# Optimization experiments

Measured on AMD Instinct MI355X. Metric: run time of the kernel, lower is better.

Reference implementation:

```python
import jax, jax.numpy as jnp
import numpy as np

B, T, C = 4, 4096, 1024
DEGREE, EXPAND = 2, 2
H = EXPAND * C  # selector / inner dim = 2048


def setup_inputs() -> dict:
    key = jax.random.key(0)
    ks = jax.random.split(key, 4)
    sc = lambda d: 1.0 / np.sqrt(d)
    return {
        "x": jax.random.normal(ks[0], (B, T, C), jnp.float32),
        "W_sel": jax.random.normal(ks[1], (C, H), jnp.float32) * sc(C),
        "W_agg": jax.random.normal(ks[2], (C, DEGREE * H), jnp.float32) * sc(C),
        "W_out": jax.random.normal(ks[3], (H, C), jnp.float32) * sc(H),
        "sqk_q": jnp.ones((H,), jnp.float32),
        "sqk_k": jnp.ones((DEGREE * H,), jnp.float32),
    }


def reference(x, W_sel, W_agg, W_out, sqk_q, sqk_k):
    # Selector branch on queries (gated): B,T,H
    s = jax.nn.silu(jnp.einsum('btc,ch->bth', x, W_sel) * sqk_q)
    # Aggregator branch on context: B,T,DEGREE*H
    h = jnp.einsum('btc,cd->btd', x, W_agg) * sqk_k
    chunks = jnp.split(h, DEGREE, axis=-1)
    # Polynomial expansion: sum_{d=1..DEGREE} prod_{k<=d} chunk_k  -> B,T,H
    p = chunks[0]
    poly = p
    for c in chunks[1:]:
        p = p * c
        poly = poly + p
    # Causal masked mean: tril(ones(T,T)) @ poly / row-count == cumsum / arange.
    # Honors the causal structure without materializing the T x T mask.
    denom = jnp.arange(1, T + 1, dtype=poly.dtype)[None, :, None]
    agg = jnp.cumsum(poly, axis=1) / denom  # B,T,H causal running mean
    # Mix selected queries with aggregated polynomial state, project out.
    return jnp.einsum('bth,hc->btc', s * agg, W_out)
```

## Files before the change

### kernel.cpp

```cpp
#include <hip/hip_runtime.h>
#include <hip/hip_bf16.h>
#include <stdint.h>

#define BB 4
#define TT 4096
#define CC 1024
#define HH 2048
#define MM (BB*TT)
#define NCK 32
#define CKS 128

using short8 = __attribute__((ext_vector_type(8))) short;
using f32x4  = __attribute__((ext_vector_type(4))) float;

__device__ __forceinline__ unsigned short f2bf(float f) {
    union { float f; uint32_t u; } v; v.f = f;
    uint32_t r = v.u + 0x7fffu + ((v.u >> 16) & 1u);
    return (unsigned short)(r >> 16);
}
__device__ __forceinline__ float bf_lo(uint32_t u) {
    union { uint32_t u; float f; } v; v.u = u << 16; return v.f;
}
__device__ __forceinline__ float bf_hi(uint32_t u) {
    union { uint32_t u; float f; } v; v.u = u & 0xFFFF0000u; return v.f;
}
__device__ __forceinline__ uint32_t pack2bf(float lo, float hi) {
    return ((uint32_t)f2bf(lo)) | (((uint32_t)f2bf(hi)) << 16);
}

__global__ void conv_x_kernel(const float* __restrict__ x, unsigned short* __restrict__ xb, int n4) {
    int i = blockIdx.x * blockDim.x + threadIdx.x;
    if (i >= n4) return;
    float4 v = ((const float4*)x)[i];
    ushort4 o;
    o.x = f2bf(v.x); o.y = f2bf(v.y); o.z = f2bf(v.z); o.w = f2bf(v.w);
    ((ushort4*)xb)[i] = o;
}

__global__ void trans_direct_kernel(const float* __restrict__ in, unsigned short* __restrict__ out,
                                    const float* __restrict__ scale, int R, int Cin) {
    __shared__ float tile[32][33];
    int c0 = blockIdx.x * 32, k0 = blockIdx.y * 32;
    int tx = threadIdx.x;
    for (int i = threadIdx.y; i < 32; i += 8) {
        float s = scale ? scale[c0 + tx] : 1.f;
        tile[i][tx] = in[(size_t)(k0 + i) * Cin + c0 + tx] * s;
    }
    __syncthreads();
    for (int i = threadIdx.y; i < 32; i += 8)
        out[(size_t)(c0 + i) * R + k0 + tx] = f2bf(tile[tx][i]);
}

__global__ void trans_pair_kernel(const float* __restrict__ in, unsigned short* __restrict__ out,
                                  const float* __restrict__ scale) {
    __shared__ float tile[32][33];
    int q0 = blockIdx.x * 32, k0 = blockIdx.y * 32;
    int g = q0 >> 5;
    int tx = threadIdx.x;
    int c = (tx < 16) ? (g * 16 + tx) : (2048 + g * 16 + tx - 16);
    float s = scale[c];
    for (int i = threadIdx.y; i < 32; i += 8)
        tile[i][tx] = in[(size_t)(k0 + i) * 4096 + c] * s;
    __syncthreads();
    for (int i = threadIdx.y; i < 32; i += 8)
        out[(size_t)(q0 + i) * 1024 + k0 + tx] = f2bf(tile[tx][i]);
}

template<int LDK, int NT>
__device__ __forceinline__ void gemm_core(
    const unsigned short* __restrict__ A,
    const unsigned short* __restrict__ Bt,
    int m0, int n0, int tid,
    f32x4 (&acc)[8][4])
{
    __shared__ __align__(16) unsigned short As[3 * 4096];
    __shared__ __align__(16) unsigned short Bs[3 * 8192];

    const int lane = tid & 63;
    const int l15  = lane & 15;
    const int quad = lane >> 4;
    const int wn   = (tid >> 6) << 6;

#pragma unroll
    for (int i = 0; i < 8; i++)
#pragma unroll
        for (int j = 0; j < 4; j++) acc[i][j] = {0.f, 0.f, 0.f, 0.f};

    const int rl  = tid >> 2;
    const int kc8 = ((tid & 3) ^ ((tid >> 3) & 3)) << 3;
    const unsigned short* gA = A  + (size_t)(m0 + rl) * LDK + kc8;
    const unsigned short* gB = Bt + (size_t)(n0 + rl) * LDK + kc8;

#define STAGE(G, L) __builtin_amdgcn_global_load_lds( \
        (const __attribute__((address_space(1))) void*)(G), \
        (__attribute__((address_space(3))) void*)(L), 16, 0, 0)
#define SWZ(row) ((quad ^ (((row) >> 1) & 3)) << 3)

#pragma unroll
    for (int t = 0; t < 2; t++) {
        STAGE(gA + t * 32,                    &As[t * 4096 + tid * 8]);
        STAGE(gA + 64 * (size_t)LDK + t * 32, &As[t * 4096 + 2048 + tid * 8]);
#pragma unroll
        for (int u = 0; u < 4; u++)
            STAGE(gB + (size_t)(u * 64) * LDK + t * 32, &Bs[t * 8192 + u * 2048 + tid * 8]);
    }
    asm volatile("s_waitcnt vmcnt(6)" ::: "memory");
    __builtin_amdgcn_s_barrier();

    unsigned short* aC = As;            unsigned short* bC = Bs;
    unsigned short* aN = As + 4096;     unsigned short* bN = Bs + 8192;
    unsigned short* aS = As + 8192;     unsigned short* bS = Bs + 16384;

    for (int t = 0; t < NT; ++t) {
        const bool pf = (t + 2) < NT;

        short8 af[4], bf[4];
#pragma unroll
        for (int i = 0; i < 4; i++) {
            int row = i * 16 + l15;
            af[i] = *(const short8*)(aC + row * 32 + SWZ(row));
        }
#pragma unroll
        for (int j = 0; j < 4; j++) {
            int row = wn + j * 16 + l15;
            bf[j] = *(const short8*)(bC + row * 32 + SWZ(row));
        }
        if (pf) {
            STAGE(gA + (size_t)(t + 2) * 32,                    aS + tid * 8);
            STAGE(gA + 64 * (size_t)LDK + (size_t)(t + 2) * 32, aS + 2048 + tid * 8);
        }
        __builtin_amdgcn_s_barrier();
        asm volatile("s_waitcnt lgkmcnt(0)" ::: "memory");
        __builtin_amdgcn_sched_barrier(0);
        __builtin_amdgcn_s_setprio(1);
#pragma unroll
        for (int i = 0; i < 4; i++)
#pragma unroll
            for (int j = 0; j < 4; j++)
                acc[i][j] = __builtin_amdgcn_mfma_f32_16x16x32_bf16(af[i], bf[j], acc[i][j], 0, 0, 0);
        __builtin_amdgcn_s_setprio(0);
        __builtin_amdgcn_sched_barrier(0);
        __builtin_amdgcn_s_barrier();

        short8 ag[4];
#pragma unroll
        for (int i = 0; i < 4; i++) {
            int row = 64 + i * 16 + l15;
            ag[i] = *(const short8*)(aC + row * 32 + SWZ(row));
        }
        if (pf) {
#pragma unroll
            for (int u = 0; u < 4; u++)
                STAGE(gB + (size_t)(u * 64) * LDK + (size_t)(t + 2) * 32, bS + u * 2048 + tid * 8);
        }
        __builtin_amdgcn_s_barrier();
        asm volatile("s_waitcnt lgkmcnt(0)" ::: "memory");
        __builtin_amdgcn_sched_barrier(0);
        __builtin_amdgcn_s_setprio(1);
#pragma unroll
        for (int i = 0; i < 4; i++)
#pragma unroll
            for (int j = 0; j < 4; j++)
                acc[4 + i][j] = __builtin_amdgcn_mfma_f32_16x16x32_bf16(ag[i], bf[j], acc[4 + i][j], 0, 0, 0);
        __builtin_amdgcn_s_setprio(0);
        __builtin_amdgcn_sched_barrier(0);
        if (t < NT - 2) { asm volatile("s_waitcnt vmcnt(6)" ::: "memory"); }
        else            { asm volatile("s_waitcnt vmcnt(0)" ::: "memory"); }
        __builtin_amdgcn_s_barrier();

        unsigned short* ta = aC; aC = aN; aN = aS; aS = ta;
        unsigned short* tb = bC; bC = bN; bN = bS; bS = tb;
    }
#undef STAGE
#undef SWZ
}

__global__ __launch_bounds__(256, 2) void gemm_fused_kernel(
    const unsigned short* __restrict__ A,
    const unsigned short* __restrict__ Bt,
    unsigned short* __restrict__ Sout,
    unsigned short* __restrict__ Pout,
    float* __restrict__ part)
{
    __shared__ float psum[128];
    const int tid = threadIdx.x;
    const int xcd = blockIdx.x & 7;
    const int j   = blockIdx.x >> 3;
    const int mt  = j / 3;
    const int nt  = xcd * 3 + (j % 3);
    const int m0 = mt << 7, n0 = nt << 8;
    if (tid < 128) psum[tid] = 0.f;

    f32x4 acc[8][4];
    gemm_core<1024, 32>(A, Bt, m0, n0, tid, acc);

    const int lane = tid & 63;
    const int l15  = lane & 15;
    const int quad = lane >> 4;
    const int wn   = (tid >> 6) << 6;

    if (nt < 8) {
#pragma unroll
        for (int i = 0; i < 8; i++)
#pragma unroll
            for (int j2 = 0; j2 < 4; j2++) {
                int col = n0 + wn + j2 * 16 + l15;
#pragma unroll
                for (int r = 0; r < 4; r++) {
                    int row = m0 + i * 16 + quad * 4 + r;
                    float v = acc[i][j2][r];
                    v = v / (1.f + __expf(-v));
                    Sout[(size_t)row * 2048 + col] = f2bf(v);
                }
            }
    } else {
        const int pbase = ((n0 - 2048 + wn) >> 1);
        float lsum0 = 0.f, lsum1 = 0.f;
#pragma unroll
        for (int i = 0; i < 8; i++) {
#pragma unroll
            for (int jp = 0; jp < 2; jp++) {
                int pcol = pbase + jp * 16 + l15;
#pragma unroll
                for (int r = 0; r < 4; r++) {
                    int row = m0 + i * 16 + quad * 4 + r;
                    float pv = acc[i][2 * jp][r] * (1.f + acc[i][2 * jp + 1][r]);
                    Pout[(size_t)row * 2048 + pcol] = f2bf(pv);
                    if (jp == 0) lsum0 += pv; else lsum1 += pv;
                }
            }
        }
        int base = (wn >> 1) + l15;
        atomicAdd(&psum[base], lsum0);
        atomicAdd(&psum[base + 16], lsum1);
        __syncthreads();
        if (tid < 128) {
            int b  = m0 >> 12;
            int ck = (m0 & 4095) >> 7;
            part[((size_t)b * NCK + ck) * 2048 + ((n0 - 2048) >> 1) + tid] = psum[tid];
        }
    }
}

__global__ __launch_bounds__(256, 2) void gemm_out_kernel(
    const unsigned short* __restrict__ A,
    const unsigned short* __restrict__ Bt,
    float* __restrict__ Cout)
{
    const int tid = threadIdx.x;
    const int xcd = blockIdx.x & 7;
    const int j   = blockIdx.x >> 3;
    const int nt  = xcd >> 1;
    const int mt  = (xcd & 1) * 64 + j;
    const int m0 = mt << 7, n0 = nt << 8;

    f32x4 acc[8][4];
    gemm_core<2048, 64>(A, Bt, m0, n0, tid, acc);

    const int lane = tid & 63;
    const int l15  = lane & 15;
    const int quad = lane >> 4;
    const int wn   = (tid >> 6) << 6;
#pragma unroll
    for (int i = 0; i < 8; i++)
#pragma unroll
        for (int j2 = 0; j2 < 4; j2++) {
            int col = n0 + wn + j2 * 16 + l15;
#pragma unroll
            for (int r = 0; r < 4; r++) {
                int row = m0 + i * 16 + quad * 4 + r;
                Cout[(size_t)row * 1024 + col] = acc[i][j2][r];
            }
        }
}

__global__ void chunk_scan_kernel(float* __restrict__ part) {
    int idx = blockIdx.x * blockDim.x + threadIdx.x;
    int b = idx >> 11, col = idx & 2047;
    float run = 0.f;
    for (int ck = 0; ck < NCK; ck++) {
        size_t off = ((size_t)b * NCK + ck) * 2048 + col;
        float v = part[off];
        part[off] = run;
        run += v;
    }
}

__global__ void finalize_kernel(unsigned short* __restrict__ poly, const unsigned short* __restrict__ s,
                                const float* __restrict__ part) {
    int seg = blockIdx.x & 3;
    int ck  = (blockIdx.x >> 2) & (NCK - 1);
    int b   = blockIdx.x >> 7;
    int cp  = seg * 256 + threadIdx.x;
    size_t po = ((size_t)b * NCK + ck) * 2048 + cp * 2;
    float run0 = part[po], run1 = part[po + 1];
    size_t base = ((size_t)b * TT + (size_t)ck * CKS) * 2048 + cp * 2;
    for (int t = 0; t < CKS; t++) {
        int tg = ck * CKS + t;
        size_t off = base + (size_t)t * 2048;
        uint32_t pv = *(const uint32_t*)&poly[off];
        run0 += bf_lo(pv);
        run1 += bf_hi(pv);
        float inv = 1.f / (float)(tg + 1);
        uint32_t sv = *(const uint32_t*)&s[off];
        float m0 = bf_lo(sv) * run0 * inv;
        float m1 = bf_hi(sv) * run1 * inv;
        *(uint32_t*)&poly[off] = pack2bf(m0, m1);
    }
}

extern "C" void kernel_launch(void* const* d_in, const int* in_sizes, int n_in,
                              void* d_out, int out_size, void* d_ws, size_t ws_size,
                              hipStream_t stream) {
    const float* x     = (const float*)d_in[0];
    const float* W_sel = (const float*)d_in[1];
    const float* W_agg = (const float*)d_in[2];
    const float* W_out = (const float*)d_in[3];
    const float* sqk_q = (const float*)d_in[4];
    const float* sqk_k = (const float*)d_in[5];
    float* out = (float*)d_out;

    char* ws = (char*)d_ws;
    unsigned short* xb    = (unsigned short*)(ws);
    unsigned short* wallT = (unsigned short*)(ws + 33554432ull);
    unsigned short* woutT = (unsigned short*)(ws + 46137344ull);
    unsigned short* s_b   = (unsigned short*)(ws + 50331648ull);
    unsigned short* poly  = (unsigned short*)(ws + 117440512ull);
    float*          part  = (float*)(ws + 184549376ull);

    dim3 tb(32, 8);
    conv_x_kernel<<<(MM * CC / 4 + 255) / 256, 256, 0, stream>>>(x, xb, MM * CC / 4);
    trans_direct_kernel<<<dim3(HH / 32, CC / 32), tb, 0, stream>>>(W_sel, wallT, sqk_q, CC, HH);
    trans_pair_kernel<<<dim3(4096 / 32, CC / 32), tb, 0, stream>>>(W_agg, wallT + 2048ull * 1024, sqk_k);
    trans_direct_kernel<<<dim3(CC / 32, HH / 32), tb, 0, stream>>>(W_out, woutT, nullptr, HH, CC);

    gemm_fused_kernel<<<(MM / 128) * 24, 256, 0, stream>>>(xb, wallT, s_b, poly, part);

    chunk_scan_kernel<<<(BB * HH) / 256, 256, 0, stream>>>(part);
    finalize_kernel<<<BB * NCK * 4, 256, 0, stream>>>(poly, s_b, part);

    gemm_out_kernel<<<(MM / 128) * (CC / 256), 256, 0, stream>>>(poly, woutT, out);
}
```

Measured before the change: 482.3 us.

## Use 256x256 tiles with 8 waves for output projection GEMM

Adds a new GEMM core with 512 threads (8 waves) computing 256x256 output tiles, using a 4-slot LDS ring with prefetch distance 2, and switches the output projection to it. Larger tiles raise arithmetic intensity and halve redundant reads of A/B per output element. The cost is 128KB of LDS per block, which limits occupancy. The XCD-aware block remapping is also dropped.

```diff
diff --git a/kernel.cpp b/kernel.cpp
--- a/kernel.cpp
+++ b/kernel.cpp
@@ -170,6 +170,112 @@
 
         unsigned short* ta = aC; aC = aN; aN = aS; aS = ta;
         unsigned short* tb = bC; bC = bN; bN = bS; bS = tb;
+    }
+#undef STAGE
+#undef SWZ
+}
+
+template<int LDK, int NT>
+__device__ __forceinline__ void gemm_core8(
+    const unsigned short* __restrict__ A,
+    const unsigned short* __restrict__ Bt,
+    int m0, int n0, int tid,
+    f32x4 (&acc)[8][4])
+{
+    __shared__ __align__(16) unsigned short As[4 * 8192];
+    __shared__ __align__(16) unsigned short Bs[4 * 8192];
+
+    const int lane = tid & 63;
+    const int wave = tid >> 6;
+    const int l15  = lane & 15;
+    const int quad = lane >> 4;
+    const int wm = (wave >> 2) << 7;
+    const int wn = (wave & 3) << 6;
+
+#pragma unroll
+    for (int i = 0; i < 8; i++)
+#pragma unroll
+        for (int j = 0; j < 4; j++) acc[i][j] = {0.f, 0.f, 0.f, 0.f};
+
+    const int rl  = tid >> 2;
+    const int kc8 = ((tid & 3) ^ ((tid >> 3) & 3)) << 3;
+    const unsigned short* gA = A  + (size_t)(m0 + rl) * LDK + kc8;
+    const unsigned short* gB = Bt + (size_t)(n0 + rl) * LDK + kc8;
+
+#define STAGE(G, L) __builtin_amdgcn_global_load_lds( \
+        (const __attribute__((address_space(1))) void*)(G), \
+        (__attribute__((address_space(3))) void*)(L), 16, 0, 0)
+#define SWZ(row) ((quad ^ (((row) >> 1) & 3)) << 3)
+
+#pragma unroll
+    for (int t = 0; t < 2; t++) {
+        STAGE(gA + t * 32,                     &As[t * 8192 + tid * 8]);
+        STAGE(gA + 128 * (size_t)LDK + t * 32, &As[t * 8192 + 4096 + tid * 8]);
+        STAGE(gB + t * 32,                     &Bs[t * 8192 + tid * 8]);
+        STAGE(gB + 128 * (size_t)LDK + t * 32, &Bs[t * 8192 + 4096 + tid * 8]);
+    }
+    asm volatile("s_waitcnt vmcnt(4)" ::: "memory");
+    __builtin_amdgcn_s_barrier();
+
+    for (int t = 0; t < NT; ++t) {
+        const unsigned short* as = &As[(t & 3) * 8192];
+        const unsigned short* bs = &Bs[(t & 3) * 8192];
+        unsigned short* asd = &As[((t + 2) & 3) * 8192];
+        unsigned short* bsd = &Bs[((t + 2) & 3) * 8192];
+        const bool pf = (t + 2) < NT;
+
+        short8 af[4], bf[4];
+#pragma unroll
+        for (int i = 0; i < 4; i++) {
+            int row = wm + i * 16 + l15;
+            af[i] = *(const short8*)(as + row * 32 + SWZ(row));
+        }
+#pragma unroll
+        for (int j = 0; j < 4; j++) {
+            int row = wn + j * 16 + l15;
+            bf[j] = *(const short8*)(bs + row * 32 + SWZ(row));
+        }
+        if (pf) {
+            STAGE(gA + (size_t)(t + 2) * 32,                     asd + tid * 8);
+            STAGE(gA + 128 * (size_t)LDK + (size_t)(t + 2) * 32, asd + 4096 + tid * 8);
+        }
+        __builtin_amdgcn_s_barrier();
+        asm volatile("s_waitcnt lgkmcnt(0)" ::: "memory");
+        __builtin_amdgcn_sched_barrier(0);
+        __builtin_amdgcn_s_setprio(1);
+#pragma unroll
+        for (int i = 0; i < 4; i++)
+#pragma unroll
+            for (int j = 0; j < 4; j++)
+                acc[i][j] = __builtin_amdgcn_mfma_f32_16x16x32_bf16(af[i], bf[j], acc[i][j], 0, 0, 0);
+        __builtin_amdgcn_s_setprio(0);
+        __builtin_amdgcn_sched_barrier(0);
+        __builtin_amdgcn_s_barrier();
+
+        short8 ag[4];
+#pragma unroll
+        for (int i = 0; i < 4; i++) {
+            int row = wm + 64 + i * 16 + l15;
+            ag[i] = *(const short8*)(as + row * 32 + SWZ(row));
+        }
+        if (pf) {
+            STAGE(gB + (size_t)(t + 2) * 32,                     bsd + tid * 8);
+            STAGE(gB + 128 * (size_t)LDK + (size_t)(t + 2) * 32, bsd + 4096 + tid * 8);
+        }
+        __builtin_amdgcn_s_barrier();
+        asm volatile("s_waitcnt lgkmcnt(0)" ::: "memory");
+        __builtin_amdgcn_sched_barrier(0);
+        __builtin_amdgcn_s_setprio(1);
+#pragma unroll
+        for (int i = 0; i < 4; i++)
+#pragma unroll
+            for (int j = 0; j < 4; j++)
+                acc[4 + i][j] = __builtin_amdgcn_mfma_f32_16x16x32_bf16(ag[i], bf[j], acc[4 + i][j], 0, 0, 0);
+        __builtin_amdgcn_s_setprio(0);
+        __builtin_amdgcn_sched_barrier(0);
+        if (t < NT - 2) { asm volatile("s_waitcnt vmcnt(4)" ::: "memory"); }
+        else            { asm volatile("s_waitcnt vmcnt(0)" ::: "memory"); }
+        __builtin_amdgcn_s_barrier();
     }
 #undef STAGE
 #undef SWZ
@@ -242,34 +348,34 @@
     }
 }
 
-__global__ __launch_bounds__(256, 2) void gemm_out_kernel(
+__global__ __launch_bounds__(512, 2) void gemm_out_kernel(
     const unsigned short* __restrict__ A,
     const unsigned short* __restrict__ Bt,
     float* __restrict__ Cout)
 {
     const int tid = threadIdx.x;
-    const int xcd = blockIdx.x & 7;
-    const int j   = blockIdx.x >> 3;
-    const int nt  = xcd >> 1;
-    const int mt  = (xcd & 1) * 64 + j;
-    const int m0 = mt << 7, n0 = nt << 8;
+    const int mt = blockIdx.x >> 2;
+    const int nt = blockIdx.x & 3;
+    const int m0 = mt << 8, n0 = nt << 8;
 
     f32x4 acc[8][4];
-    gemm_core<2048, 64>(A, Bt, m0, n0, tid, acc);
+    gemm_core8<2048, 64>(A, Bt, m0, n0, tid, acc);
 
     const int lane = tid & 63;
+    const int wave = tid >> 6;
     const int l15  = lane & 15;
     const int quad = lane >> 4;
-    const int wn   = (tid >> 6) << 6;
+    const int wm = (wave >> 2) << 7;
+    const int wn = (wave & 3) << 6;
 #pragma unroll
     for (int i = 0; i < 8; i++)
 #pragma unroll
-        for (int j2 = 0; j2 < 4; j2++) {
-            int col = n0 + wn + j2 * 16 + l15;
+        for (int j = 0; j < 4; j++) {
+            int col = n0 + wn + j * 16 + l15;
 #pragma unroll
             for (int r = 0; r < 4; r++) {
-                int row = m0 + i * 16 + quad * 4 + r;
-                Cout[(size_t)row * 1024 + col] = acc[i][j2][r];
+                int row = m0 + wm + i * 16 + quad * 4 + r;
+                Cout[(size_t)row * 1024 + col] = acc[i][j][r];
             }
         }
 }
@@ -339,5 +445,5 @@
     chunk_scan_kernel<<<(BB * HH) / 256, 256, 0, stream>>>(part);
     finalize_kernel<<<BB * NCK * 4, 256, 0, stream>>>(poly, s_b, part);
 
-    gemm_out_kernel<<<(MM / 128) * (CC / 256), 256, 0, stream>>>(poly, woutT, out);
-}
+    gemm_out_kernel<<<(MM / 256) * (CC / 256), 512, 0, stream>>>(poly, woutT, out);
+}
```

After: 483.3 us. No clear change (+0.2%).
